# Performance work log

Measured on AMD Instinct MI355X. Metric: run time of the kernel, lower is better.

The kernel has to match this reference:

```python
import jax, jax.numpy as jnp
import numpy as np
from jax import lax

WINDOW_SIZE = 11
SIGMA = 1.5
C1 = 0.01 ** 2
C2 = 0.03 ** 2


def _gaussian_window(window_size: int, sigma: float) -> jnp.ndarray:
    coords = jnp.arange(window_size, dtype=jnp.float32) - window_size // 2
    g = jnp.exp(-0.5 * (coords / sigma) ** 2)
    g = g / g.sum()
    return g[:, None] * g[None, :]  # (ws, ws)


def _dwconv(x, win2d):
    # x: (B, C, H, W); win2d: (ws, ws). Depthwise conv, same padding.
    c = x.shape[1]
    ws = win2d.shape[0]
    pad = ws // 2
    k = jnp.broadcast_to(win2d[None, None], (c, 1, ws, ws))  # (O=C, I/g=1, ws, ws)
    return lax.conv_general_dilated(
        x, k, window_strides=(1, 1), padding=[(pad, pad), (pad, pad)],
        dimension_numbers=('NCHW', 'OIHW', 'NCHW'), feature_group_count=c)


def setup_inputs() -> dict:
    key = jax.random.key(0)
    k1, k2 = jax.random.split(key)
    shape = (32, 3, 512, 512)
    img1 = jax.random.uniform(k1, shape, dtype=jnp.float32)
    img2 = jax.random.uniform(k2, shape, dtype=jnp.float32)
    return {"img1": img1, "img2": img2}


def reference(img1, img2):
    win = _gaussian_window(WINDOW_SIZE, SIGMA).astype(img1.dtype)
    mu1 = _dwconv(img1, win)
    mu2 = _dwconv(img2, win)
    mu1_sq = mu1 * mu1
    mu2_sq = mu2 * mu2
    mu12 = mu1 * mu2
    sigma1_sq = _dwconv(img1 * img1, win) - mu1_sq
    sigma2_sq = _dwconv(img2 * img2, win) - mu2_sq
    sigma12 = _dwconv(img1 * img2, win) - mu12
    numerator = (2.0 * mu12 + C1) * (2.0 * sigma12 + C2)
    denominator = (mu1_sq + mu2_sq + C1) * (sigma1_sq + sigma2_sq + C2)
    ssim_map = numerator / denominator
    return 1.0 - ssim_map.mean()
```

## Files before the change

kernel.cpp:

```cpp
#include <hip/hip_runtime.h>
#include <hip/hip_fp16.h>

#define IMG   512
#define TW    32
#define TH    64
#define WS    11
#define NP    96
#define NSLOT 256
#define PR2   37
#define RSTR  32
#define PLANE (PR2*RSTR)

typedef __attribute__((ext_vector_type(2))) _Float16 half2v;

static __device__ __forceinline__ uint pkh(float ev, float od) {
    return __builtin_bit_cast(uint, __builtin_amdgcn_cvt_pkrtz(ev, od));
}
static __device__ __forceinline__ ushort f2h(float x) {
    return __builtin_bit_cast(ushort, (_Float16)x);
}
static __device__ __forceinline__ float h2f(ushort u) {
    return (float)__builtin_bit_cast(_Float16, u);
}

__global__ __launch_bounds__(256, 4) void ssim_main(const float* __restrict__ img1,
                                                    const float* __restrict__ img2,
                                                    double* __restrict__ acc) {
    constexpr float W[WS] = {
        0.00102837990674f, 0.00759883148699f, 0.03600079242909f,
        0.10936069869137f, 0.21300538108707f, 0.26601190869814f,
        0.21300538108707f, 0.10936069869137f, 0.03600079242909f,
        0.00759883148699f, 0.00102837990674f };

    __shared__ uint HP[5 * PLANE];

    const int tid = threadIdx.x;
    const int bx = blockIdx.x;
    const int by = blockIdx.y;
    const float* p1 = img1 + (size_t)blockIdx.z * (IMG * IMG);
    const float* p2 = img2 + (size_t)blockIdx.z * (IMG * IMG);

    ushort us[12];
    #pragma unroll
    for (int t = 0; t < WS; ++t) us[t] = f2h(W[t]);
    us[11] = 0;
    float alpha = 0.f;
    #pragma unroll
    for (int t = 0; t < WS; ++t) alpha += h2f(us[t]);
    uint pe[6], po[6];
    #pragma unroll
    for (int j = 0; j < 6; ++j) {
        pe[j] = (uint)us[2*j] | ((uint)us[2*j+1] << 16);
        po[j] = (j ? (uint)us[2*j-1] : 0u) | ((uint)us[2*j] << 16);
    }

    for (int u = tid; u < PR2 * 8; u += 256) {
        const int pr = u >> 3;
        const int cg = u & 7;

        float A[5][2][4];
        #pragma unroll
        for (int s = 0; s < 5; ++s)
            #pragma unroll
            for (int rw = 0; rw < 2; ++rw)
                #pragma unroll
                for (int o = 0; o < 4; ++o) A[s][rw][o] = 0.f;

        #pragma unroll
        for (int rw = 0; rw < 2; ++rw) {
            const int gy = by * TH + 2 * pr + rw - 5;
            const bool rowOK = (unsigned)gy < IMG;
            const float* r1 = p1 + (size_t)gy * IMG;
            const float* r2 = p2 + (size_t)gy * IMG;
            #pragma unroll
            for (int j = 0; j < 5; ++j) {
                const int gx = bx * TW + cg * 4 - 8 + 4 * j;
                float4 X = make_float4(0.f,0.f,0.f,0.f), Y = X;
                if (rowOK && (unsigned)gx < IMG) {
                    X = *(const float4*)(r1 + gx);
                    Y = *(const float4*)(r2 + gx);
                }
                const float e1[4] = {X.x,X.y,X.z,X.w};
                const float e2[4] = {Y.x,Y.y,Y.z,Y.w};
                #pragma unroll
                for (int e = 0; e < 4; ++e) {
                    const int i = 4*j + e;
                    if (i < 3 || i > 16) continue;
                    const float x1 = e1[e], x2 = e2[e];
                    const float q11 = x1*x1, q22 = x2*x2, q12 = x1*x2;
                    #pragma unroll
                    for (int o = 0; o < 4; ++o) {
                        const int t = i - 3 - o;
                        if (t >= 0 && t < WS) {
                            A[0][rw][o] += W[t]*x1;  A[1][rw][o] += W[t]*x2;
                            A[2][rw][o] += W[t]*q11; A[3][rw][o] += W[t]*q22;
                            A[4][rw][o] += W[t]*q12;
                        }
                    }
                }
            }
        }

        #pragma unroll
        for (int s = 0; s < 5; ++s) {
            const uint4 pv = make_uint4(pkh(A[s][0][0], A[s][1][0]),
                                        pkh(A[s][0][1], A[s][1][1]),
                                        pkh(A[s][0][2], A[s][1][2]),
                                        pkh(A[s][0][3], A[s][1][3]));
            *(uint4*)&HP[(s * PR2 + pr) * RSTR + cg * 4] = pv;
        }
    }
    __syncthreads();

    const int q0 = tid >> 3;
    const int cg = tid & 7;

    float m[5][2][4];
    #pragma unroll
    for (int s = 0; s < 5; ++s)
        #pragma unroll
        for (int pth = 0; pth < 2; ++pth)
            #pragma unroll
            for (int c = 0; c < 4; ++c) m[s][pth][c] = 0.f;

    #pragma unroll
    for (int s = 0; s < 5; ++s) {
        #pragma unroll
        for (int j = 0; j <= 5; ++j) {
            const uint4 v = *(const uint4*)&HP[(s * PR2 + q0 + j) * RSTR + cg * 4];
            const uint vv[4] = {v.x, v.y, v.z, v.w};
            #pragma unroll
            for (int c = 0; c < 4; ++c) {
                asm("v_dot2_f32_f16 %0, %1, %2, %0"
                    : "+v"(m[s][0][c]) : "v"(vv[c]), "v"(pe[j]));
                asm("v_dot2_f32_f16 %0, %1, %2, %0"
                    : "+v"(m[s][1][c]) : "v"(vv[c]), "v"(po[j]));
            }
        }
    }

    const float invA = 1.0f / alpha;
    const float C1 = 0.01f*0.01f, C2 = 0.03f*0.03f;
    float lsum = 0.f;
    #pragma unroll
    for (int pth = 0; pth < 2; ++pth) {
        #pragma unroll
        for (int c = 0; c < 4; ++c) {
            const float mu1 = m[0][pth][c] * invA, mu2 = m[1][pth][c] * invA;
            const float m11 = m[2][pth][c] * invA, m22 = m[3][pth][c] * invA;
            const float m12 = m[4][pth][c] * invA;
            const float mu1s = mu1*mu1, mu2s = mu2*mu2, mu12 = mu1*mu2;
            const float s11 = m11 - mu1s;
            const float s22 = m22 - mu2s;
            const float s12 = m12 - mu12;
            const float num = (2.f*mu12 + C1) * (2.f*s12 + C2);
            const float den = (mu1s + mu2s + C1) * (s11 + s22 + C2);
            lsum += num * __builtin_amdgcn_rcpf(den);
        }
    }

    #pragma unroll
    for (int d = 32; d >= 1; d >>= 1)
        lsum += __shfl_down(lsum, d, 64);
    __shared__ float wsum[4];
    if ((tid & 63) == 0) wsum[tid >> 6] = lsum;
    __syncthreads();
    if (tid == 0) {
        const float t = wsum[0] + wsum[1] + wsum[2] + wsum[3];
        const int bid = (blockIdx.z * gridDim.y + blockIdx.y) * gridDim.x + blockIdx.x;
        atomicAdd(&acc[bid & (NSLOT - 1)], (double)t);
    }
}

__global__ void ssim_final(const double* __restrict__ acc, float* __restrict__ out) {
    const int l = threadIdx.x;
    double s = acc[l] + acc[l + 64] + acc[l + 128] + acc[l + 192];
    #pragma unroll
    for (int d = 32; d >= 1; d >>= 1)
        s += __shfl_down(s, d, 64);
    if (l == 0)
        out[0] = 1.0f - (float)(s / (double)((size_t)NP * IMG * IMG));
}

extern "C" void kernel_launch(void* const* d_in, const int* in_sizes, int n_in,
                              void* d_out, int out_size, void* d_ws, size_t ws_size,
                              hipStream_t stream) {
    const float* img1 = (const float*)d_in[0];
    const float* img2 = (const float*)d_in[1];
    float* out = (float*)d_out;
    double* acc = (double*)d_ws;

    hipMemsetAsync(d_ws, 0, NSLOT * sizeof(double), stream);

    dim3 grid(IMG / TW, IMG / TH, NP);
    ssim_main<<<grid, dim3(256), 0, stream>>>(img1, img2, acc);
    ssim_final<<<1, dim3(64), 0, stream>>>(acc, out);
}
```

Measured before the change: 106.7 us.

## Compute horizontal Gaussian pass with MFMA on fp16 Toeplitz weights

Replaces the scalar FMA horizontal convolution stage with 32x32x16 fp16 MFMA instructions. Three waves each load 32 image rows, pack them to fp16 and multiply against a banded Toeplitz matrix built from the fp16 window weights, which turns the horizontal pass into matrix multiplies. Products are squared and multiplied in packed fp16 before the MFMA, and the weights are now normalised by alpha squared. The goal is to offload the arithmetic-heavy first pass to the matrix cores. In exchange, fp16 squaring of the inputs reduces precision, and one of the four waves sits idle during this stage.

```diff
diff --git a/kernel.cpp b/kernel.cpp
--- a/kernel.cpp
+++ b/kernel.cpp
@@ -11,10 +11,12 @@
 #define RSTR  32
 #define PLANE (PR2*RSTR)
 
-typedef __attribute__((ext_vector_type(2))) _Float16 half2v;
-
-static __device__ __forceinline__ uint pkh(float ev, float od) {
-    return __builtin_bit_cast(uint, __builtin_amdgcn_cvt_pkrtz(ev, od));
+typedef _Float16 f16x8 __attribute__((ext_vector_type(8)));
+typedef float    f32x16 __attribute__((ext_vector_type(16)));
+typedef _Float16 h2v   __attribute__((ext_vector_type(2)));
+
+static __device__ __forceinline__ uint pkh(float a, float b) {
+    return __builtin_bit_cast(uint, __builtin_amdgcn_cvt_pkrtz(a, b));
 }
 static __device__ __forceinline__ ushort f2h(float x) {
     return __builtin_bit_cast(ushort, (_Float16)x);
@@ -22,6 +24,13 @@
 static __device__ __forceinline__ float h2f(ushort u) {
     return (float)__builtin_bit_cast(_Float16, u);
 }
+static __device__ __forceinline__ uint pkmul(uint a, uint b) {
+    const h2v r = __builtin_bit_cast(h2v, a) * __builtin_bit_cast(h2v, b);
+    return __builtin_bit_cast(uint, r);
+}
+
+#define DOT(ACC, VW, WT) \
+    asm("v_dot2_f32_f16 %0, %1, %2, %0" : "+v"(ACC) : "v"(VW), "v"(WT))
 
 __global__ __launch_bounds__(256, 4) void ssim_main(const float* __restrict__ img1,
                                                     const float* __restrict__ img2,
@@ -34,7 +43,10 @@
 
     __shared__ uint HP[5 * PLANE];
 
-    const int tid = threadIdx.x;
+    const int tid  = threadIdx.x;
+    const int wid  = tid >> 6;
+    const int col  = tid & 31;
+    const int h    = (tid >> 5) & 1;
     const int bx = blockIdx.x;
     const int by = blockIdx.y;
     const float* p1 = img1 + (size_t)blockIdx.z * (IMG * IMG);
@@ -54,60 +66,67 @@
         po[j] = (j ? (uint)us[2*j-1] : 0u) | ((uint)us[2*j] << 16);
     }
 
-    for (int u = tid; u < PR2 * 8; u += 256) {
-        const int pr = u >> 3;
-        const int cg = u & 7;
-
-        float A[5][2][4];
-        #pragma unroll
-        for (int s = 0; s < 5; ++s)
-            #pragma unroll
-            for (int rw = 0; rw < 2; ++rw)
+    if (wid < 3) {
+        const int rbBase   = (wid == 0) ? 0 : (wid == 1) ? 32 : 42;
+        const int pairBase = rbBase >> 1;
+        const int gy = by * TH + rbBase + col - 5;
+        const bool rowOK = (unsigned)gy < IMG;
+        const float* r1 = p1 + (size_t)gy * IMG;
+        const float* r2 = p2 + (size_t)gy * IMG;
+
+        uint xw[2][3][4];
+        #pragma unroll
+        for (int T = 0; T < 3; ++T) {
+            const int gx0 = bx * TW - 8 + 16 * T + 8 * h;
+            float4 qa = make_float4(0.f,0.f,0.f,0.f), qb = qa, qc = qa, qd = qa;
+            if (rowOK && (unsigned)gx0 < IMG)       { qa = *(const float4*)(r1 + gx0);     qc = *(const float4*)(r2 + gx0); }
+            if (rowOK && (unsigned)(gx0 + 4) < IMG) { qb = *(const float4*)(r1 + gx0 + 4); qd = *(const float4*)(r2 + gx0 + 4); }
+            xw[0][T][0] = pkh(qa.x,qa.y); xw[0][T][1] = pkh(qa.z,qa.w);
+            xw[0][T][2] = pkh(qb.x,qb.y); xw[0][T][3] = pkh(qb.z,qb.w);
+            xw[1][T][0] = pkh(qc.x,qc.y); xw[1][T][1] = pkh(qc.z,qc.w);
+            xw[1][T][2] = pkh(qd.x,qd.y); xw[1][T][3] = pkh(qd.z,qd.w);
+        }
+
+        uint Bw[3][4];
+        #pragma unroll
+        for (int T = 0; T < 3; ++T) {
+            #pragma unroll
+            for (int w4 = 0; w4 < 4; ++w4) {
+                const int t0 = 16*T + 8*h + 2*w4 - col - 3;
+                ushort b0 = 0, b1 = 0;
                 #pragma unroll
-                for (int o = 0; o < 4; ++o) A[s][rw][o] = 0.f;
-
-        #pragma unroll
-        for (int rw = 0; rw < 2; ++rw) {
-            const int gy = by * TH + 2 * pr + rw - 5;
-            const bool rowOK = (unsigned)gy < IMG;
-            const float* r1 = p1 + (size_t)gy * IMG;
-            const float* r2 = p2 + (size_t)gy * IMG;
-            #pragma unroll
-            for (int j = 0; j < 5; ++j) {
-                const int gx = bx * TW + cg * 4 - 8 + 4 * j;
-                float4 X = make_float4(0.f,0.f,0.f,0.f), Y = X;
-                if (rowOK && (unsigned)gx < IMG) {
-                    X = *(const float4*)(r1 + gx);
-                    Y = *(const float4*)(r2 + gx);
+                for (int t = 0; t < WS; ++t) {
+                    if (t0 == t)     b0 = us[t];
+                    if (t0 + 1 == t) b1 = us[t];
                 }
-                const float e1[4] = {X.x,X.y,X.z,X.w};
-                const float e2[4] = {Y.x,Y.y,Y.z,Y.w};
-                #pragma unroll
-                for (int e = 0; e < 4; ++e) {
-                    const int i = 4*j + e;
-                    if (i < 3 || i > 16) continue;
-                    const float x1 = e1[e], x2 = e2[e];
-                    const float q11 = x1*x1, q22 = x2*x2, q12 = x1*x2;
-                    #pragma unroll
-                    for (int o = 0; o < 4; ++o) {
-                        const int t = i - 3 - o;
-                        if (t >= 0 && t < WS) {
-                            A[0][rw][o] += W[t]*x1;  A[1][rw][o] += W[t]*x2;
-                            A[2][rw][o] += W[t]*q11; A[3][rw][o] += W[t]*q22;
-                            A[4][rw][o] += W[t]*q12;
-                        }
-                    }
-                }
+                Bw[T][w4] = (uint)b0 | ((uint)b1 << 16);
             }
         }
 
         #pragma unroll
         for (int s = 0; s < 5; ++s) {
-            const uint4 pv = make_uint4(pkh(A[s][0][0], A[s][1][0]),
-                                        pkh(A[s][0][1], A[s][1][1]),
-                                        pkh(A[s][0][2], A[s][1][2]),
-                                        pkh(A[s][0][3], A[s][1][3]));
-            *(uint4*)&HP[(s * PR2 + pr) * RSTR + cg * 4] = pv;
+            f32x16 a = {};
+            #pragma unroll
+            for (int T = 0; T < 3; ++T) {
+                union { uint u[4]; f16x8 v; } A, B;
+                if      (s == 0) { A.u[0]=xw[0][T][0]; A.u[1]=xw[0][T][1]; A.u[2]=xw[0][T][2]; A.u[3]=xw[0][T][3]; }
+                else if (s == 1) { A.u[0]=xw[1][T][0]; A.u[1]=xw[1][T][1]; A.u[2]=xw[1][T][2]; A.u[3]=xw[1][T][3]; }
+                else if (s == 2) { A.u[0]=pkmul(xw[0][T][0],xw[0][T][0]); A.u[1]=pkmul(xw[0][T][1],xw[0][T][1]);
+                                   A.u[2]=pkmul(xw[0][T][2],xw[0][T][2]); A.u[3]=pkmul(xw[0][T][3],xw[0][T][3]); }
+                else if (s == 3) { A.u[0]=pkmul(xw[1][T][0],xw[1][T][0]); A.u[1]=pkmul(xw[1][T][1],xw[1][T][1]);
+                                   A.u[2]=pkmul(xw[1][T][2],xw[1][T][2]); A.u[3]=pkmul(xw[1][T][3],xw[1][T][3]); }
+                else             { A.u[0]=pkmul(xw[0][T][0],xw[1][T][0]); A.u[1]=pkmul(xw[0][T][1],xw[1][T][1]);
+                                   A.u[2]=pkmul(xw[0][T][2],xw[1][T][2]); A.u[3]=pkmul(xw[0][T][3],xw[1][T][3]); }
+                B.u[0]=Bw[T][0]; B.u[1]=Bw[T][1]; B.u[2]=Bw[T][2]; B.u[3]=Bw[T][3];
+                a = __builtin_amdgcn_mfma_f32_32x32x16_f16(A.v, B.v, a, 0, 0, 0);
+            }
+            #pragma unroll
+            for (int r = 0; r < 8; ++r) {
+                constexpr int plist[8] = {0,1,4,5,8,9,12,13};
+                const uint wpk = pkh(a[2*r], a[2*r+1]);
+                const int p = plist[r] + 2*h + pairBase;
+                HP[(s * PR2 + p) * RSTR + col] = wpk;
+            }
         }
     }
     __syncthreads();
@@ -131,24 +150,23 @@
             const uint vv[4] = {v.x, v.y, v.z, v.w};
             #pragma unroll
             for (int c = 0; c < 4; ++c) {
-                asm("v_dot2_f32_f16 %0, %1, %2, %0"
-                    : "+v"(m[s][0][c]) : "v"(vv[c]), "v"(pe[j]));
-                asm("v_dot2_f32_f16 %0, %1, %2, %0"
-                    : "+v"(m[s][1][c]) : "v"(vv[c]), "v"(po[j]));
+                DOT(m[s][0][c], vv[c], pe[j]);
+                DOT(m[s][1][c], vv[c], po[j]);
             }
         }
     }
 
     const float invA = 1.0f / alpha;
+    const float invA2 = invA * invA;
     const float C1 = 0.01f*0.01f, C2 = 0.03f*0.03f;
     float lsum = 0.f;
     #pragma unroll
     for (int pth = 0; pth < 2; ++pth) {
         #pragma unroll
         for (int c = 0; c < 4; ++c) {
-            const float mu1 = m[0][pth][c] * invA, mu2 = m[1][pth][c] * invA;
-            const float m11 = m[2][pth][c] * invA, m22 = m[3][pth][c] * invA;
-            const float m12 = m[4][pth][c] * invA;
+            const float mu1 = m[0][pth][c] * invA2, mu2 = m[1][pth][c] * invA2;
+            const float m11 = m[2][pth][c] * invA2, m22 = m[3][pth][c] * invA2;
+            const float m12 = m[4][pth][c] * invA2;
             const float mu1s = mu1*mu1, mu2s = mu2*mu2, mu12 = mu1*mu2;
             const float s11 = m11 - mu1s;
             const float s22 = m22 - mu2s;
```

New measurement: 130.6 us. 22.5% more time.
